# Optimization experiments

Measured on AMD Instinct MI355X. Metric: run time of the kernel, lower is better.

Reference implementation:

```python
import jax, jax.numpy as jnp
import numpy as np

STRIDE = 1
KSIZE = 3
DEMOD = True


def _conv_single(xi, wi, pad):
    # xi: [C,H,W], wi: [O,C,k,k] -> [O,H,W]
    out = jax.lax.conv_general_dilated(
        xi[None], wi, window_strides=(STRIDE, STRIDE),
        padding=[(pad, pad), (pad, pad)],
        dimension_numbers=("NCHW", "OIHW", "NCHW"))
    return out[0]


def setup_inputs() -> dict:
    key = jax.random.key(0)
    ks = jax.random.split(key, 6)
    B, Cin, Cout, S, H, W = 8, 512, 512, 512, 64, 64
    return {
        "x": jax.random.normal(ks[0], (B, Cin, H, W), jnp.float32),
        "y": jax.random.normal(ks[1], (B, S), jnp.float32),
        "affine_w": jax.random.normal(ks[2], (Cin, S), jnp.float32) * 0.02,
        "affine_b": jax.random.normal(ks[3], (Cin,), jnp.float32) * 0.02,
        "weight": jax.random.normal(ks[4], (Cout, Cin, KSIZE, KSIZE), jnp.float32) * 0.05,
        "bias": jax.random.normal(ks[5], (1, Cout, 1, 1), jnp.float32) * 0.02,
    }


def reference(x, y, affine_w, affine_b, weight, bias):
    B, _, H, W = x.shape
    style_dim = affine_w.shape[1]
    coef = 1.0 / np.sqrt(style_dim)  # ELR: gain / sqrt(fan_in)
    # style modulation scale per input channel: [B, Cin]
    s = (y * coef) @ affine_w.T + affine_b + 1.0
    # per-sample weights: [B, O, I, k, k]
    w = weight[None, :, :, :, :] * s[:, None, :, None, None]
    if DEMOD:
        d = jax.lax.rsqrt(jnp.sum(w * w, axis=(2, 3, 4), keepdims=True) + 1e-4)
        w = w * d
    pad = ((H - 1) * (STRIDE - 1) + (KSIZE - 1)) // 2
    out = jax.vmap(lambda xi, wi: _conv_single(xi, wi, pad))(x, w)  # [B,O,H,W]
    return out + bias
```

## Files before the change

kernel.cpp:

```cpp
#include <hip/hip_runtime.h>

typedef __attribute__((ext_vector_type(8))) short short8;
typedef __attribute__((ext_vector_type(4))) float floatx4;
typedef unsigned short u16;
typedef unsigned int u32;

#define NB 8
#define CI 512
#define CO 512
#define HH 64
#define WW 64
#define HP 66
#define WP 66
#define BK 64

__device__ __forceinline__ u16 f2bf(float f) {
  u32 u = __builtin_bit_cast(u32, f);
  u += 0x7fffu + ((u >> 16) & 1u);
  return (u16)(u >> 16);
}

__device__ __forceinline__ void gload16(const void* g, void* l) {
  __builtin_amdgcn_global_load_lds(
      (const __attribute__((address_space(1))) unsigned int*)g,
      (__attribute__((address_space(3))) unsigned int*)l, 16, 0, 0);
}

__global__ __launch_bounds__(256) void k_style(
    const float* __restrict__ y, const float* __restrict__ aw,
    const float* __restrict__ ab, float* __restrict__ s)
{
  const int wid = blockIdx.x * 4 + (threadIdx.x >> 6);
  const int lane = threadIdx.x & 63;
  const int b = wid >> 9, i = wid & 511;
  float sum = 0.f;
  #pragma unroll
  for (int j = 0; j < 8; ++j) {
    const int k = lane + (j << 6);
    sum += y[b * CI + k] * aw[i * CI + k];
  }
  #pragma unroll
  for (int off = 32; off; off >>= 1) sum += __shfl_xor(sum, off);
  if (lane == 0) s[wid] = sum * 0.044194173824159216f + ab[i] + 1.0f;
}

__global__ __launch_bounds__(256) void k_wprep(
    const float* __restrict__ wt, float* __restrict__ wsum, u16* __restrict__ wbv)
{
  const int idx = blockIdx.x * 256 + threadIdx.x;
  const int i = idx & 511;
  const int o = idx >> 9;
  const float* p = wt + (size_t)idx * 9;
  float v[9];
  float sum = 0.f;
  #pragma unroll
  for (int t = 0; t < 9; ++t) { v[t] = p[t]; sum += v[t] * v[t]; }
  wsum[idx] = sum;
  #pragma unroll
  for (int t = 0; t < 9; ++t) wbv[(((o * 9 + t) << 9) | i)] = f2bf(v[t]);
}

__global__ __launch_bounds__(256) void k_demod(
    const float* __restrict__ wsum, const float* __restrict__ s,
    float* __restrict__ d)
{
  const int wid = blockIdx.x * 4 + (threadIdx.x >> 6);
  const int lane = threadIdx.x & 63;
  const int b = wid >> 9, o = wid & 511;
  float sum = 0.f;
  #pragma unroll
  for (int j = 0; j < 8; ++j) {
    const int i = lane + (j << 6);
    const float sv = s[b * CI + i];
    sum += wsum[o * CI + i] * sv * sv;
  }
  #pragma unroll
  for (int off = 32; off; off >>= 1) sum += __shfl_xor(sum, off);
  if (lane == 0) d[wid] = rsqrtf(sum + 1e-4f);
}

__global__ __launch_bounds__(256) void k_xform(
    const float* __restrict__ x, const float* __restrict__ s,
    u16* __restrict__ xs)
{
  __shared__ __align__(16) u16 lds[64 * 72];
  const int blk = blockIdx.x;
  const int ic = blk & 7;
  const int h = (blk >> 3) & 63;
  const int b = blk >> 9;
  const int i0 = ic << 6;
  const int t = threadIdx.x;
  const int w = t & 63;
  const int i4 = t >> 6;
  #pragma unroll
  for (int p = 0; p < 16; ++p) {
    const int ii = i4 + (p << 2);
    const float xv = x[((size_t)(b * CI + i0 + ii) * HH + h) * WW + w];
    const float sv = s[b * CI + i0 + ii];
    lds[w * 72 + ii] = f2bf(xv * sv);
  }
  const uint4 z4 = {0u, 0u, 0u, 0u};
  if (t < 16) {
    const int wside = (t < 8) ? 0 : 65;
    const int q = t & 7;
    *(uint4*)&xs[((size_t)(b * HP + h + 1) * WP + wside) * CI + i0 + (q << 3)] = z4;
  }
  if (h == 0) {
    for (int idx = t; idx < 2 * 66 * 8; idx += 256) {
      const int row = (idx < 528) ? 0 : 65;
      const int rem = (idx < 528) ? idx : idx - 528;
      const int wz = rem >> 3;
      const int q = rem & 7;
      *(uint4*)&xs[((size_t)(b * HP + row) * WP + wz) * CI + i0 + (q << 3)] = z4;
    }
  }
  __syncthreads();
  const int w2 = t >> 2;
  const int q = t & 3;
  const uint4* src = (const uint4*)&lds[w2 * 72 + (q << 4)];
  const uint4 v0 = src[0];
  const uint4 v1 = src[1];
  u16* dst = xs + ((size_t)(b * HP + h + 1) * WP + (w2 + 1)) * CI + i0 + (q << 4);
  *(uint4*)dst = v0;
  *((uint4*)dst + 1) = v1;
}

__global__ __launch_bounds__(512, 2) void k_conv(
    const u16* __restrict__ xs, const u16* __restrict__ wb,
    const float* __restrict__ dmod, const float* __restrict__ bias,
    float* __restrict__ out)
{
  __shared__ __align__(16) u16 lA[2 * 16384];
  __shared__ __align__(16) u16 lB[2 * 16384];

  const int blk = blockIdx.x;
  const int nt = blk & 15;
  const int mt = (blk >> 4) & 1;
  const int b  = blk >> 5;
  const int ob = mt << 8;
  const int p0 = nt << 8;

  const int tid = threadIdx.x;
  const int wid = tid >> 6;
  const int lane = tid & 63;
  const int col = lane & 15;
  const int k8  = lane >> 4;
  const int wr  = wid >> 2;
  const int wc  = wid & 3;

  const int lr = lane >> 3;
  const int ls = lane & 7;
  const int swz = ls ^ lr;

  u32 aoffs[4], boffs[4], ldst[4];
  #pragma unroll
  for (int g = 0; g < 4; ++g) {
    const int rg = (wid << 5) + (g << 3);
    aoffs[g] = (u32)((ob + rg + lr) * 4608 + (swz << 3));
    const int p = p0 + rg + lr;
    boffs[g] = (u32)(((b * HP + (p >> 6)) * WP + (p & 63)) * 512 + (swz << 3));
    ldst[g] = (u32)(rg << 6);
  }

  const u32 sA0 = (u32)(((0 + k8) ^ (col & 7)) << 3);
  const u32 sA1 = (u32)(((4 + k8) ^ (col & 7)) << 3);
  const u32 aRead = (u32)((((wr << 7) + col) << 6));
  const u32 bRead = (u32)((((wc << 6) + col) << 6));

  floatx4 acc[8][4];
  #pragma unroll
  for (int m = 0; m < 8; ++m)
    #pragma unroll
    for (int n = 0; n < 4; ++n)
      acc[m][n] = (floatx4){0.f, 0.f, 0.f, 0.f};

  short8 a0[4][2], b0[2][2], b1[2][2];

#define STAGE_B(KC, C) do {                                                   \
    const int kc2_ = (KC);                                                    \
    const int tap_ = kc2_ >> 3;                                               \
    const int kh_ = tap_ / 3;                                                 \
    const int kw_ = tap_ - kh_ * 3;                                           \
    const u32 bt_ = (u32)(((kh_ * WP + kw_) << 9) + ((kc2_ & 7) << 6));       \
    _Pragma("unroll")                                                         \
    for (int g = 0; g < 4; ++g)                                               \
      gload16(xs + boffs[g] + bt_, &lB[((C) << 14) + ldst[g]]);               \
  } while (0)

#define STAGE_A(KC, C) do {                                                   \
    const u32 at_ = (u32)((KC) << 6);                                         \
    _Pragma("unroll")                                                         \
    for (int g = 0; g < 4; ++g)                                               \
      gload16(wb + aoffs[g] + at_, &lA[((C) << 14) + ldst[g]]);               \
  } while (0)

#define READ_A(PA, MH) do {                                                   \
    _Pragma("unroll")                                                         \
    for (int mq = 0; mq < 4; ++mq) {                                          \
      a0[mq][0] = *(const short8*)((PA) + (MH) * 4096 + mq * 1024 + sA0);     \
      a0[mq][1] = *(const short8*)((PA) + (MH) * 4096 + mq * 1024 + sA1);     \
    }                                                                         \
  } while (0)

#define READ_B(PB, NH, BV) do {                                               \
    _Pragma("unroll")                                                         \
    for (int nq = 0; nq < 2; ++nq) {                                          \
      BV[nq][0] = *(const short8*)((PB) + (NH) * 2048 + nq * 1024 + sA0);     \
      BV[nq][1] = *(const short8*)((PB) + (NH) * 2048 + nq * 1024 + sA1);     \
    }                                                                         \
  } while (0)

#define MFMA_Q(MH, NH, BV) do {                                               \
    _Pragma("unroll")                                                         \
    for (int kk = 0; kk < 2; ++kk)                                            \
      _Pragma("unroll")                                                       \
      for (int nq = 0; nq < 2; ++nq)                                          \
        _Pragma("unroll")                                                     \
        for (int mq = 0; mq < 4; ++mq)                                        \
          acc[(MH)*4+mq][(NH)*2+nq] = __builtin_amdgcn_mfma_f32_16x16x32_bf16(\
              a0[mq][kk], BV[nq][kk], acc[(MH)*4+mq][(NH)*2+nq], 0, 0, 0);    \
  } while (0)

#define BODY(T, DOSTAGE, WMODE) do {                                          \
    const int c_ = (T) & 1;                                                   \
    const u16* pA = lA + (c_ << 14) + aRead;                                  \
    const u16* pB = lB + (c_ << 14) + bRead;                                  \
                          \
    READ_A(pA, 0);                                                            \
    READ_B(pB, 0, b0);                                                        \
    READ_B(pB, 1, b1);                                                        \
    __builtin_amdgcn_s_barrier();                                             \
    __builtin_amdgcn_s_setprio(1);                                            \
    MFMA_Q(0, 0, b0); MFMA_Q(0, 1, b1);                                       \
    __builtin_amdgcn_s_setprio(0);                                            \
    __builtin_amdgcn_s_barrier();                                             \
       \
    __builtin_amdgcn_sched_barrier(0);                                        \
    if (DOSTAGE) STAGE_B((T) + 2, c_);                                        \
    READ_A(pA, 1);                                                            \
    __builtin_amdgcn_s_barrier();                                             \
    __builtin_amdgcn_s_setprio(1); MFMA_Q(1, 1, b1); __builtin_amdgcn_s_setprio(0); \
    __builtin_amdgcn_s_barrier();                                             \
     \
    __builtin_amdgcn_sched_barrier(0);                                        \
    if (DOSTAGE) STAGE_A((T) + 2, c_);                                        \
    __builtin_amdgcn_s_setprio(1); MFMA_Q(1, 0, b0); __builtin_amdgcn_s_setprio(0); \
    if (WMODE == 1)      asm volatile("s_waitcnt vmcnt(8)" ::: "memory");     \
    else if (WMODE == 2) asm volatile("s_waitcnt vmcnt(0)" ::: "memory");     \
    if (WMODE != 0) __builtin_amdgcn_s_barrier();                             \
  } while (0)

  STAGE_B(0, 0); STAGE_A(0, 0);
  STAGE_B(1, 1); STAGE_A(1, 1);
  asm volatile("s_waitcnt vmcnt(8)" ::: "memory");
  __builtin_amdgcn_sched_barrier(0);
  __builtin_amdgcn_s_barrier();

  for (int t = 0; t < 70; ++t) BODY(t, 1, 1);
  BODY(70, 0, 2);
  BODY(71, 0, 0);

#undef STAGE_B
#undef STAGE_A
#undef READ_A
#undef READ_B
#undef MFMA_Q
#undef BODY

  #pragma unroll
  for (int m = 0; m < 8; ++m) {
    #pragma unroll
    for (int r = 0; r < 4; ++r) {
      const int o = ob + (wr << 7) + (m << 4) + (k8 << 2) + r;
      const float dm = dmod[b * CO + o];
      const float bs = bias[o];
      float* po = out + (((size_t)(b * CO + o)) << 12) + p0 + (wc << 6);
      #pragma unroll
      for (int n = 0; n < 4; ++n)
        po[(n << 4) + col] = acc[m][n][r] * dm + bs;
    }
  }
}

extern "C" void kernel_launch(void* const* d_in, const int* in_sizes, int n_in,
                              void* d_out, int out_size, void* d_ws, size_t ws_size,
                              hipStream_t stream) {
  const float* x    = (const float*)d_in[0];
  const float* y    = (const float*)d_in[1];
  const float* aw   = (const float*)d_in[2];
  const float* ab   = (const float*)d_in[3];
  const float* wt   = (const float*)d_in[4];
  const float* bias = (const float*)d_in[5];
  float* out = (float*)d_out;

  char* ws = (char*)d_ws;
  const size_t XS_BYTES = (size_t)NB * HP * WP * CI * 2;
  const size_t WB_BYTES = (size_t)CO * 9 * CI * 2;
  const size_t WS_BYTES = (size_t)CO * CI * 4;
  u16* xsb    = (u16*)ws;
  u16* wbuf   = (u16*)(ws + XS_BYTES);
  float* wsum = (float*)(ws + XS_BYTES + WB_BYTES);
  float* sbuf = (float*)(ws + XS_BYTES + WB_BYTES + WS_BYTES);
  float* dbuf = sbuf + NB * CI;

  k_style<<<dim3(1024), dim3(256), 0, stream>>>(y, aw, ab, sbuf);
  k_wprep<<<dim3(1024), dim3(256), 0, stream>>>(wt, wsum, wbuf);
  k_demod<<<dim3(1024), dim3(256), 0, stream>>>(wsum, sbuf, dbuf);
  k_xform<<<dim3(4096), dim3(256), 0, stream>>>(x, sbuf, xsb);
  k_conv <<<dim3(256), dim3(512), 0, stream>>>(xsb, wbuf, dbuf, bias, out);
}
```

Before: 163.7 us.

## Restructure main loop into 8-phase schedule with split A/B staging

Reworks the K-loop pipeline of the bf16 MFMA implicit-GEMM convolution. Each iteration now covers two K-tiles in eight barrier-separated phases. The A and B global-to-LDS loads are split into half-tile chunks interleaved between MFMA quarters, and A is staged one tile ahead while B is staged two ahead. The per-thread staging rows are also remapped. The aim is to spread memory traffic evenly across the compute phases and keep fewer loads in flight per wait. The cost is more barriers per tile, plus a risk of LDS buffer reuse hazards from the tighter A prefetch distance.

```diff
diff --git a/kernel.cpp b/kernel.cpp
--- a/kernel.cpp
+++ b/kernel.cpp
@@ -152,14 +152,15 @@
   const int ls = lane & 7;
   const int swz = ls ^ lr;
 
-  u32 aoffs[4], boffs[4], ldst[4];
-  #pragma unroll
-  for (int g = 0; g < 4; ++g) {
-    const int rg = (wid << 5) + (g << 3);
-    aoffs[g] = (u32)((ob + rg + lr) * 4608 + (swz << 3));
-    const int p = p0 + rg + lr;
-    boffs[g] = (u32)(((b * HP + (p >> 6)) * WP + (p & 63)) * 512 + (swz << 3));
-    ldst[g] = (u32)(rg << 6);
+  u32 aoff[4], boff[4], ldst[4];
+  #pragma unroll
+  for (int h2 = 0; h2 < 4; ++h2) {
+    const int rowBase = ((h2 >> 1) << 7) + (wid << 4) + ((h2 & 1) << 3);
+    const int rowIdx = rowBase + lr;
+    aoff[h2] = (u32)((ob + rowIdx) * 4608 + (swz << 3));
+    const int p = p0 + rowIdx;
+    boff[h2] = (u32)(((b * HP + (p >> 6)) * WP + (p & 63)) * 512 + (swz << 3));
+    ldst[h2] = (u32)(rowBase << 6);
   }
 
   const u32 sA0 = (u32)(((0 + k8) ^ (col & 7)) << 3);
@@ -176,22 +177,20 @@
 
   short8 a0[4][2], b0[2][2], b1[2][2];
 
-#define STAGE_B(KC, C) do {                                                   \
-    const int kc2_ = (KC);                                                    \
-    const int tap_ = kc2_ >> 3;                                               \
+#define SA(TILE, H, BUF) do {                                                 \
+    const u32 at_ = (u32)((TILE) << 6);                                       \
+    gload16(wb + aoff[(H)*2+0] + at_, &lA[((BUF) << 14) + ldst[(H)*2+0]]);    \
+    gload16(wb + aoff[(H)*2+1] + at_, &lA[((BUF) << 14) + ldst[(H)*2+1]]);    \
+  } while (0)
+
+#define SB(TILE, H, BUF) do {                                                 \
+    const int t_ = (TILE);                                                    \
+    const int tap_ = t_ >> 3;                                                 \
     const int kh_ = tap_ / 3;                                                 \
     const int kw_ = tap_ - kh_ * 3;                                           \
-    const u32 bt_ = (u32)(((kh_ * WP + kw_) << 9) + ((kc2_ & 7) << 6));       \
-    _Pragma("unroll")                                                         \
-    for (int g = 0; g < 4; ++g)                                               \
-      gload16(xs + boffs[g] + bt_, &lB[((C) << 14) + ldst[g]]);               \
-  } while (0)
-
-#define STAGE_A(KC, C) do {                                                   \
-    const u32 at_ = (u32)((KC) << 6);                                         \
-    _Pragma("unroll")                                                         \
-    for (int g = 0; g < 4; ++g)                                               \
-      gload16(wb + aoffs[g] + at_, &lA[((C) << 14) + ldst[g]]);               \
+    const u32 bt_ = (u32)(((kh_ * WP + kw_) << 9) + ((t_ & 7) << 6));         \
+    gload16(xs + boff[(H)*2+0] + bt_, &lB[((BUF) << 14) + ldst[(H)*2+0]]);    \
+    gload16(xs + boff[(H)*2+1] + bt_, &lB[((BUF) << 14) + ldst[(H)*2+1]]);    \
   } while (0)
 
 #define READ_A(PA, MH) do {                                                   \
@@ -221,51 +220,72 @@
               a0[mq][kk], BV[nq][kk], acc[(MH)*4+mq][(NH)*2+nq], 0, 0, 0);    \
   } while (0)
 
-#define BODY(T, DOSTAGE, WMODE) do {                                          \
-    const int c_ = (T) & 1;                                                   \
-    const u16* pA = lA + (c_ << 14) + aRead;                                  \
-    const u16* pB = lB + (c_ << 14) + bRead;                                  \
+#define SBAR __builtin_amdgcn_s_barrier()
+#define SCH0 __builtin_amdgcn_sched_barrier(0)
+#define PRI1 __builtin_amdgcn_s_setprio(1)
+#define PRI0 __builtin_amdgcn_s_setprio(0)
+
+#define BODY8(T0, FULL) do {                                                  \
+    const u16* pA0 = lA + aRead;                                              \
+    const u16* pB0 = lB + bRead;                                              \
+    const u16* pA1 = lA + 16384 + aRead;                                      \
+    const u16* pB1 = lB + 16384 + bRead;                                      \
+                                        \
+    READ_A(pA0, 0); READ_B(pB0, 0, b0);                                       \
+    SCH0; SA((T0) + 1, 0, 1);                                                 \
+    SBAR; PRI1; MFMA_Q(0, 0, b0); PRI0; SBAR;                                 \
+                                                          \
+    READ_B(pB0, 1, b1);                                                       \
+    SCH0; SA((T0) + 1, 1, 1);                                                 \
+    SBAR; PRI1; MFMA_Q(0, 1, b1); PRI0; SBAR;                                 \
+                           \
+    READ_A(pA0, 1);                                                           \
+    SCH0; if (FULL) SB((T0) + 2, 0, 0);                                       \
+    SBAR; PRI1; MFMA_Q(1, 1, b1); PRI0; SBAR;                                 \
                           \
-    READ_A(pA, 0);                                                            \
-    READ_B(pB, 0, b0);                                                        \
-    READ_B(pB, 1, b1);                                                        \
-    __builtin_amdgcn_s_barrier();                                             \
-    __builtin_amdgcn_s_setprio(1);                                            \
-    MFMA_Q(0, 0, b0); MFMA_Q(0, 1, b1);                                       \
-    __builtin_amdgcn_s_setprio(0);                                            \
-    __builtin_amdgcn_s_barrier();                                             \
+    SCH0; if (FULL) SB((T0) + 2, 1, 0);                                       \
+    SBAR; PRI1; MFMA_Q(1, 0, b0); PRI0;                                       \
+    if (FULL) asm volatile("s_waitcnt vmcnt(4)" ::: "memory");                \
+    else      asm volatile("s_waitcnt vmcnt(0)" ::: "memory");                \
+    SBAR;                                                                     \
        \
-    __builtin_amdgcn_sched_barrier(0);                                        \
-    if (DOSTAGE) STAGE_B((T) + 2, c_);                                        \
-    READ_A(pA, 1);                                                            \
-    __builtin_amdgcn_s_barrier();                                             \
-    __builtin_amdgcn_s_setprio(1); MFMA_Q(1, 1, b1); __builtin_amdgcn_s_setprio(0); \
-    __builtin_amdgcn_s_barrier();                                             \
-     \
-    __builtin_amdgcn_sched_barrier(0);                                        \
-    if (DOSTAGE) STAGE_A((T) + 2, c_);                                        \
-    __builtin_amdgcn_s_setprio(1); MFMA_Q(1, 0, b0); __builtin_amdgcn_s_setprio(0); \
-    if (WMODE == 1)      asm volatile("s_waitcnt vmcnt(8)" ::: "memory");     \
-    else if (WMODE == 2) asm volatile("s_waitcnt vmcnt(0)" ::: "memory");     \
-    if (WMODE != 0) __builtin_amdgcn_s_barrier();                             \
-  } while (0)
-
-  STAGE_B(0, 0); STAGE_A(0, 0);
-  STAGE_B(1, 1); STAGE_A(1, 1);
-  asm volatile("s_waitcnt vmcnt(8)" ::: "memory");
-  __builtin_amdgcn_sched_barrier(0);
-  __builtin_amdgcn_s_barrier();
-
-  for (int t = 0; t < 70; ++t) BODY(t, 1, 1);
-  BODY(70, 0, 2);
-  BODY(71, 0, 0);
-
-#undef STAGE_B
-#undef STAGE_A
+    READ_A(pA1, 0); READ_B(pB1, 0, b0);                                       \
+    SCH0; if (FULL) SA((T0) + 2, 0, 0);                                       \
+    SBAR; PRI1; MFMA_Q(0, 0, b0); PRI0; SBAR;                                 \
+                                                          \
+    READ_B(pB1, 1, b1);                                                       \
+    SCH0; if (FULL) SA((T0) + 2, 1, 0);                                       \
+    SBAR; PRI1; MFMA_Q(0, 1, b1); PRI0; SBAR;                                 \
+                           \
+    READ_A(pA1, 1);                                                           \
+    SCH0; if (FULL) SB((T0) + 3, 0, 1);                                       \
+    SBAR; PRI1; MFMA_Q(1, 1, b1); PRI0; SBAR;                                 \
+                          \
+    SCH0; if (FULL) SB((T0) + 3, 1, 1);                                       \
+    SBAR; PRI1; MFMA_Q(1, 0, b0); PRI0;                                       \
+    if (FULL) asm volatile("s_waitcnt vmcnt(4)" ::: "memory");                \
+    SBAR;                                                                     \
+  } while (0)
+
+  SB(0, 0, 0); SB(0, 1, 0); SA(0, 0, 0); SA(0, 1, 0);
+  SB(1, 0, 1); SB(1, 1, 1);
+  asm volatile("s_waitcnt vmcnt(4)" ::: "memory");
+  SCH0;
+  SBAR;
+
+  for (int j = 0; j < 35; ++j) BODY8(j * 2, 1);
+  BODY8(70, 0);
+
+#undef SA
+#undef SB
 #undef READ_A
 #undef READ_B
 #undef MFMA_Q
-#undef BODY
+#undef BODY8
+#undef SBAR
+#undef SCH0
+#undef PRI1
+#undef PRI0
 
   #pragma unroll
   for (int m = 0; m < 8; ++m) {
```

Result: faster. 157.4 us (-3.9%).

## Retile implicit-GEMM conv to 256x128 tiles with BK=32 and swizzled block order

Applied to the files above, without the earlier changes.

The conv kernel moves from 512-thread blocks with 256x256 output tiles and a 64-wide K step to 256-thread blocks with 256x128 tiles and a 32-wide K step, which doubles the grid to 512 blocks and quarters LDS per block. The LDS layout switches from XOR swizzling to a 4-slot rotation, and block indices are remapped so that blocks sharing weights or inputs are scheduled close together. The aim is more resident blocks and better L2 locality. The cost is lower arithmetic intensity per tile, twice as many K iterations, and more barrier overhead.

```diff
diff --git a/kernel.cpp b/kernel.cpp
--- a/kernel.cpp
+++ b/kernel.cpp
@@ -12,7 +12,6 @@
 #define WW 64
 #define HP 66
 #define WP 66
-#define BK 64
 
 __device__ __forceinline__ u16 f2bf(float f) {
   u32 u = __builtin_bit_cast(u32, f);
@@ -125,47 +124,53 @@
   *((uint4*)dst + 1) = v1;
 }
 
-__global__ __launch_bounds__(512, 2) void k_conv(
+__global__ __launch_bounds__(256, 2) void k_conv(
     const u16* __restrict__ xs, const u16* __restrict__ wb,
     const float* __restrict__ dmod, const float* __restrict__ bias,
     float* __restrict__ out)
 {
-  __shared__ __align__(16) u16 lA[2 * 16384];
-  __shared__ __align__(16) u16 lB[2 * 16384];
-
-  const int blk = blockIdx.x;
-  const int nt = blk & 15;
-  const int mt = (blk >> 4) & 1;
-  const int b  = blk >> 5;
+  __shared__ __align__(16) u16 lA[2 * 8192];
+  __shared__ __align__(16) u16 lB[2 * 4096];
+
+  const int blk0 = blockIdx.x;
+  const int blk = (blk0 & 7) * 64 + (blk0 >> 3);
+  const int nt = blk & 31;
+  const int mt = (blk >> 5) & 1;
+  const int b  = blk >> 6;
   const int ob = mt << 8;
-  const int p0 = nt << 8;
+  const int p0 = nt << 7;
 
   const int tid = threadIdx.x;
   const int wid = tid >> 6;
   const int lane = tid & 63;
   const int col = lane & 15;
   const int k8  = lane >> 4;
-  const int wr  = wid >> 2;
-  const int wc  = wid & 3;
-
-  const int lr = lane >> 3;
-  const int ls = lane & 7;
-  const int swz = ls ^ lr;
-
-  u32 aoffs[4], boffs[4], ldst[4];
+  const int wr  = wid >> 1;
+  const int wc  = wid & 1;
+
+  const int rot4 = (lane >> 3) & 3;
+  const int sslot = ((lane & 3) - rot4) & 3;
+  const int rowin = lane >> 2;
+
+  u32 aoffs[4], aldst[4];
   #pragma unroll
   for (int g = 0; g < 4; ++g) {
-    const int rg = (wid << 5) + (g << 3);
-    aoffs[g] = (u32)((ob + rg + lr) * 4608 + (swz << 3));
-    const int p = p0 + rg + lr;
-    boffs[g] = (u32)(((b * HP + (p >> 6)) * WP + (p & 63)) * 512 + (swz << 3));
-    ldst[g] = (u32)(rg << 6);
-  }
-
-  const u32 sA0 = (u32)(((0 + k8) ^ (col & 7)) << 3);
-  const u32 sA1 = (u32)(((4 + k8) ^ (col & 7)) << 3);
-  const u32 aRead = (u32)((((wr << 7) + col) << 6));
-  const u32 bRead = (u32)((((wc << 6) + col) << 6));
+    const int row = wid * 64 + g * 16 + rowin;
+    aoffs[g] = (u32)((ob + row) * 4608 + sslot * 8);
+    aldst[g] = (u32)((wid * 4 + g) * 512 + lane * 8);
+  }
+  u32 boffs[2], bldst[2];
+  #pragma unroll
+  for (int g = 0; g < 2; ++g) {
+    const int row = wid * 32 + g * 16 + rowin;
+    const int p = p0 + row;
+    boffs[g] = (u32)(((b * HP + (p >> 6)) * WP + (p & 63)) * 512 + sslot * 8);
+    bldst[g] = (u32)((wid * 2 + g) * 512 + lane * 8);
+  }
+
+  const u32 rdslot = (u32)(((k8 + (col >> 1)) & 3) * 8);
+  const u32 aRead = (u32)((wr * 128 + col) * 32) + rdslot;
+  const u32 bRead = (u32)((wc * 64 + col) * 32) + rdslot;
 
   floatx4 acc[8][4];
   #pragma unroll
@@ -174,98 +179,76 @@
     for (int n = 0; n < 4; ++n)
       acc[m][n] = (floatx4){0.f, 0.f, 0.f, 0.f};
 
-  short8 a0[4][2], b0[2][2], b1[2][2];
-
-#define STAGE_B(KC, C) do {                                                   \
-    const int kc2_ = (KC);                                                    \
-    const int tap_ = kc2_ >> 3;                                               \
+  short8 av[8], bv[4];
+
+#define STAGE(T, BUF) do {                                                    \
+    const int t_ = (T);                                                       \
+    const int tap_ = t_ >> 4;                                                 \
     const int kh_ = tap_ / 3;                                                 \
     const int kw_ = tap_ - kh_ * 3;                                           \
-    const u32 bt_ = (u32)(((kh_ * WP + kw_) << 9) + ((kc2_ & 7) << 6));       \
+    const u32 at_ = (u32)(t_ << 5);                                           \
+    const u32 bt_ = (u32)(((kh_ * WP + kw_) << 9) + ((t_ & 15) << 5));        \
     _Pragma("unroll")                                                         \
     for (int g = 0; g < 4; ++g)                                               \
-      gload16(xs + boffs[g] + bt_, &lB[((C) << 14) + ldst[g]]);               \
-  } while (0)
-
-#define STAGE_A(KC, C) do {                                                   \
-    const u32 at_ = (u32)((KC) << 6);                                         \
-    _Pragma("unroll")                                                         \
-    for (int g = 0; g < 4; ++g)                                               \
-      gload16(wb + aoffs[g] + at_, &lA[((C) << 14) + ldst[g]]);               \
-  } while (0)
-
-#define READ_A(PA, MH) do {                                                   \
-    _Pragma("unroll")                                                         \
-    for (int mq = 0; mq < 4; ++mq) {                                          \
-      a0[mq][0] = *(const short8*)((PA) + (MH) * 4096 + mq * 1024 + sA0);     \
-      a0[mq][1] = *(const short8*)((PA) + (MH) * 4096 + mq * 1024 + sA1);     \
-    }                                                                         \
-  } while (0)
-
-#define READ_B(PB, NH, BV) do {                                               \
-    _Pragma("unroll")                                                         \
-    for (int nq = 0; nq < 2; ++nq) {                                          \
-      BV[nq][0] = *(const short8*)((PB) + (NH) * 2048 + nq * 1024 + sA0);     \
-      BV[nq][1] = *(const short8*)((PB) + (NH) * 2048 + nq * 1024 + sA1);     \
-    }                                                                         \
-  } while (0)
-
-#define MFMA_Q(MH, NH, BV) do {                                               \
-    _Pragma("unroll")                                                         \
-    for (int kk = 0; kk < 2; ++kk)                                            \
+      gload16(wb + aoffs[g] + at_, &lA[((BUF) << 13) + aldst[g]]);            \
+    _Pragma("unroll")                                                         \
+    for (int g = 0; g < 2; ++g)                                               \
+      gload16(xs + boffs[g] + bt_, &lB[((BUF) << 12) + bldst[g]]);            \
+  } while (0)
+
+#define READS(BUF) do {                                                       \
+    const u16* pA = lA + ((BUF) << 13) + aRead;                               \
+    const u16* pB = lB + ((BUF) << 12) + bRead;                               \
+    _Pragma("unroll")                                                         \
+    for (int m = 0; m < 8; ++m) av[m] = *(const short8*)(pA + m * 512);       \
+    _Pragma("unroll")                                                         \
+    for (int n = 0; n < 4; ++n) bv[n] = *(const short8*)(pB + n * 512);       \
+  } while (0)
+
+#define MFMA_H(H) do {                                                        \
+    _Pragma("unroll")                                                         \
+    for (int n = 0; n < 4; ++n)                                               \
       _Pragma("unroll")                                                       \
-      for (int nq = 0; nq < 2; ++nq)                                          \
-        _Pragma("unroll")                                                     \
-        for (int mq = 0; mq < 4; ++mq)                                        \
-          acc[(MH)*4+mq][(NH)*2+nq] = __builtin_amdgcn_mfma_f32_16x16x32_bf16(\
-              a0[mq][kk], BV[nq][kk], acc[(MH)*4+mq][(NH)*2+nq], 0, 0, 0);    \
-  } while (0)
-
-#define BODY(T, DOSTAGE, WMODE) do {                                          \
-    const int c_ = (T) & 1;                                                   \
-    const u16* pA = lA + (c_ << 14) + aRead;                                  \
-    const u16* pB = lB + (c_ << 14) + bRead;                                  \
-                          \
-    READ_A(pA, 0);                                                            \
-    READ_B(pB, 0, b0);                                                        \
-    READ_B(pB, 1, b1);                                                        \
-    __builtin_amdgcn_s_barrier();                                             \
-    __builtin_amdgcn_s_setprio(1);                                            \
-    MFMA_Q(0, 0, b0); MFMA_Q(0, 1, b1);                                       \
-    __builtin_amdgcn_s_setprio(0);                                            \
-    __builtin_amdgcn_s_barrier();                                             \
-       \
-    __builtin_amdgcn_sched_barrier(0);                                        \
-    if (DOSTAGE) STAGE_B((T) + 2, c_);                                        \
-    READ_A(pA, 1);                                                            \
-    __builtin_amdgcn_s_barrier();                                             \
-    __builtin_amdgcn_s_setprio(1); MFMA_Q(1, 1, b1); __builtin_amdgcn_s_setprio(0); \
-    __builtin_amdgcn_s_barrier();                                             \
-     \
-    __builtin_amdgcn_sched_barrier(0);                                        \
-    if (DOSTAGE) STAGE_A((T) + 2, c_);                                        \
-    __builtin_amdgcn_s_setprio(1); MFMA_Q(1, 0, b0); __builtin_amdgcn_s_setprio(0); \
-    if (WMODE == 1)      asm volatile("s_waitcnt vmcnt(8)" ::: "memory");     \
+      for (int m = 0; m < 4; ++m)                                             \
+        acc[(H)*4+m][n] = __builtin_amdgcn_mfma_f32_16x16x32_bf16(            \
+            av[(H)*4+m], bv[n], acc[(H)*4+m][n], 0, 0, 0);                    \
+  } while (0)
+
+#define SBAR __builtin_amdgcn_s_barrier()
+#define SCH0 __builtin_amdgcn_sched_barrier(0)
+
+#define TILE(T, BUF, DOSTAGE, WMODE) do {                                     \
+    READS(BUF);                                                               \
+    SBAR;                                                                     \
+    __builtin_amdgcn_s_setprio(1); MFMA_H(0); __builtin_amdgcn_s_setprio(0);  \
+    asm volatile("s_waitcnt lgkmcnt(0)" ::: "memory");                        \
+    SBAR;                                                                     \
+    SCH0;                                                                     \
+    if (DOSTAGE) STAGE((T) + 2, BUF);                                         \
+    __builtin_amdgcn_s_setprio(1); MFMA_H(1); __builtin_amdgcn_s_setprio(0);  \
+    if (WMODE == 1)      asm volatile("s_waitcnt vmcnt(6)" ::: "memory");     \
     else if (WMODE == 2) asm volatile("s_waitcnt vmcnt(0)" ::: "memory");     \
-    if (WMODE != 0) __builtin_amdgcn_s_barrier();                             \
-  } while (0)
-
-  STAGE_B(0, 0); STAGE_A(0, 0);
-  STAGE_B(1, 1); STAGE_A(1, 1);
-  asm volatile("s_waitcnt vmcnt(8)" ::: "memory");
-  __builtin_amdgcn_sched_barrier(0);
-  __builtin_amdgcn_s_barrier();
-
-  for (int t = 0; t < 70; ++t) BODY(t, 1, 1);
-  BODY(70, 0, 2);
-  BODY(71, 0, 0);
-
-#undef STAGE_B
-#undef STAGE_A
-#undef READ_A
-#undef READ_B
-#undef MFMA_Q
-#undef BODY
+    if (WMODE != 0) SBAR;                                                     \
+  } while (0)
+
+  STAGE(0, 0);
+  STAGE(1, 1);
+  asm volatile("s_waitcnt vmcnt(6)" ::: "memory");
+  SBAR;
+
+  for (int j = 0; j < 71; ++j) {
+    TILE(2 * j,     0, 1, 1);
+    TILE(2 * j + 1, 1, 1, 1);
+  }
+  TILE(142, 0, 0, 2);
+  TILE(143, 1, 0, 0);
+
+#undef STAGE
+#undef READS
+#undef MFMA_H
+#undef TILE
+#undef SBAR
+#undef SCH0
 
   #pragma unroll
   for (int m = 0; m < 8; ++m) {
@@ -307,5 +290,5 @@
   k_wprep<<<dim3(1024), dim3(256), 0, stream>>>(wt, wsum, wbuf);
   k_demod<<<dim3(1024), dim3(256), 0, stream>>>(wsum, sbuf, dbuf);
   k_xform<<<dim3(4096), dim3(256), 0, stream>>>(x, sbuf, xsb);
-  k_conv <<<dim3(256), dim3(512), 0, stream>>>(xsb, wbuf, dbuf, bias, out);
-}
+  k_conv <<<dim3(512), dim3(256), 0, stream>>>(xsb, wbuf, dbuf, bias, out);
+}
```

Result: slower. 189.5 us (+15.8%).
